# Kernel tuning notes

Measured on AMD Instinct MI355X. Metric: run time of the kernel, lower is better.

The kernel has to match this reference:

```python
import jax, jax.numpy as jnp
import numpy as np

N_USER = 100000
N_ITEM = 50000
N_NODES = N_USER + N_ITEM
LATDIM = 64
N_EDGES = 4800000
N_LAYERS = 3


def setup_inputs() -> dict:
    key = jax.random.key(0)
    k1, k2, k3, k4 = jax.random.split(key, 4)
    ini_embeds = jax.random.normal(k1, (N_NODES, LATDIM), dtype=jnp.float32)
    edge_src = jax.random.randint(k2, (N_EDGES,), 0, N_NODES, dtype=jnp.int32)
    edge_dst = jax.random.randint(k3, (N_EDGES,), 0, N_NODES, dtype=jnp.int32)
    edge_w = jax.random.uniform(k4, (N_EDGES,), dtype=jnp.float32)
    return {
        "ini_embeds": ini_embeds,
        "edge_src": edge_src,
        "edge_dst": edge_dst,
        "edge_w": edge_w,
        "n_user": N_USER,
        "n_layers": N_LAYERS,
    }


def _spmm(edge_src, edge_dst, edge_w, x, n_nodes):
    # out[dst] += w * x[src]  == adj @ x for sparse adj in COO form
    msgs = x[edge_src] * edge_w[:, None]  # [E, D]
    return jax.ops.segment_sum(msgs, edge_dst, num_segments=n_nodes)


def reference(ini_embeds, edge_src, edge_dst, edge_w, n_user, n_layers):
    n_nodes = ini_embeds.shape[0]
    embeds = ini_embeds
    acc = ini_embeds  # running sum of all layer embeddings (LightGCN layer sum)
    for _ in range(n_layers):
        embeds = _spmm(edge_src, edge_dst, edge_w, embeds, n_nodes)
        acc = acc + embeds
    return acc[:n_user], acc[n_user:]
```

## Files before the change

### kernel.cpp

```cpp
#include <hip/hip_runtime.h>
#include <hip/hip_fp16.h>


#define D 64
#define BSH 9
#define BW 512
#define PTILE 16384

#define MIXLO(acc, reg, w) \
    asm("v_fma_mix_f32 %0, %1, %2, %0 op_sel:[0,0,0] op_sel_hi:[1,0,0]" \
        : "+v"(acc) : "v"(reg), "v"(w))
#define MIXHI(acc, reg, w) \
    asm("v_fma_mix_f32 %0, %1, %2, %0 op_sel:[1,0,0] op_sel_hi:[1,0,0]" \
        : "+v"(acc) : "v"(reg), "v"(w))

__global__ __launch_bounds__(1024) void lg_tilehist(const int* __restrict__ edst,
                                                    int* __restrict__ tcnt,
                                                    int E, int NB, int ntiles,
                                                    const float* __restrict__ ini,
                                                    __half* __restrict__ h0, int n4) {
    extern __shared__ int cnt[];
    int t = blockIdx.x;
    int lo = t * PTILE;
    int hi = lo + PTILE; if (hi > E) hi = E;
    for (int i = threadIdx.x; i < NB; i += 1024) cnt[i] = 0;
    __syncthreads();
    for (int i = lo + threadIdx.x; i < hi; i += 1024)
        atomicAdd(&cnt[edst[i] >> BSH], 1);
    __syncthreads();
    for (int b = threadIdx.x; b < NB; b += 1024)
        tcnt[b * ntiles + t] = cnt[b];
    const float4* src = (const float4*)ini;
    uint2* dst = (uint2*)h0;
    int gst = gridDim.x * 1024;
    for (int i = blockIdx.x * 1024 + threadIdx.x; i < n4; i += gst) {
        float4 v = src[i];
        __half2 a = __floats2half2_rn(v.x, v.y);
        __half2 b = __floats2half2_rn(v.z, v.w);
        uint2 u;
        u.x = *reinterpret_cast<unsigned int*>(&a);
        u.y = *reinterpret_cast<unsigned int*>(&b);
        dst[i] = u;
    }
}

__global__ __launch_bounds__(1024) void lg_scan1(const int* __restrict__ tcnt,
                                                 int* __restrict__ tbase,
                                                 int* __restrict__ blksum, int NT) {
    __shared__ int lds[1024];
    int tid = threadIdx.x;
    int i = blockIdx.x * 1024 + tid;
    int v = (i < NT) ? tcnt[i] : 0;
    lds[tid] = v;
    __syncthreads();
    for (int off = 1; off < 1024; off <<= 1) {
        int t = (tid >= off) ? lds[tid - off] : 0;
        __syncthreads();
        lds[tid] += t;
        __syncthreads();
    }
    if (i < NT) tbase[i] = lds[tid] - v;
    if (tid == 1023) blksum[blockIdx.x] = lds[tid];
}

__global__ __launch_bounds__(128) void lg_scan2(int* __restrict__ blksum, int nblk,
                                                int* __restrict__ rowptr, int n_nodes, int E) {
    __shared__ int lds[128];
    int tid = threadIdx.x;
    int v = (tid < nblk) ? blksum[tid] : 0;
    lds[tid] = v;
    __syncthreads();
    for (int off = 1; off < 128; off <<= 1) {
        int t = (tid >= off) ? lds[tid - off] : 0;
        __syncthreads();
        lds[tid] += t;
        __syncthreads();
    }
    if (tid < nblk) blksum[tid] = lds[tid] - v;
    if (tid == 0) rowptr[n_nodes] = E;
}

__global__ __launch_bounds__(1024) void lg_scatter2(const int* __restrict__ esrc,
                                                    const int* __restrict__ edst,
                                                    const float* __restrict__ ew,
                                                    const int* __restrict__ tbase,
                                                    const int* __restrict__ blksum,
                                                    int2* __restrict__ bbuf,
                                                    int E, int NB, int ntiles) {
    extern __shared__ int cur[];
    int t = blockIdx.x;
    int lo = t * PTILE;
    int hi = lo + PTILE; if (hi > E) hi = E;
    for (int b = threadIdx.x; b < NB; b += 1024) {
        int idx = b * ntiles + t;
        cur[b] = tbase[idx] + blksum[idx >> 10];
    }
    __syncthreads();
    for (int i = lo + threadIdx.x; i < hi; i += 1024) {
        int d = edst[i];
        int b = d >> BSH;
        int p = atomicAdd(&cur[b], 1);
        bbuf[p] = make_int2(esrc[i] | ((d & (BW - 1)) << 18), __float_as_int(ew[i]));
    }
}

__global__ __launch_bounds__(1024) void lg_bfinal(const int2* __restrict__ bbuf,
                                                  const int* __restrict__ tbase,
                                                  const int* __restrict__ blksum,
                                                  unsigned int* __restrict__ edata,
                                                  int* __restrict__ rowptr,
                                                  int n_nodes, int NB, int ntiles, int E) {
    __shared__ int cnt[BW];
    __shared__ int cur[BW];
    __shared__ int psum[BW];
    int b = blockIdx.x;
    int i0 = b * ntiles;
    int s = tbase[i0] + blksum[i0 >> 10];
    int e;
    if (b == NB - 1) e = E;
    else { int i1 = (b + 1) * ntiles; e = tbase[i1] + blksum[i1 >> 10]; }
    int tid = threadIdx.x;
    if (tid < BW) cnt[tid] = 0;
    __syncthreads();
    for (int i = s + tid; i < e; i += 1024)
        atomicAdd(&cnt[((unsigned)bbuf[i].x >> 18) & (BW - 1)], 1);
    __syncthreads();
    if (tid < BW) psum[tid] = cnt[tid];
    __syncthreads();
    for (int off = 1; off < BW; off <<= 1) {
        int v = 0;
        if (tid < BW && tid >= off) v = psum[tid - off];
        __syncthreads();
        if (tid < BW) psum[tid] += v;
        __syncthreads();
    }
    if (tid < BW) {
        int excl = psum[tid] - cnt[tid];
        cur[tid] = excl;
        int node = b * BW + tid;
        if (node < n_nodes) rowptr[node] = s + excl;
    }
    __syncthreads();
    for (int i = s + tid; i < e; i += 1024) {
        int2 ed = bbuf[i];
        int loc = ((unsigned)ed.x >> 18) & (BW - 1);
        int p = s + atomicAdd(&cur[loc], 1);
        unsigned int src = (unsigned)(ed.x & 0x3FFFF);
        float w = __int_as_float(ed.y);
        unsigned int wq = (unsigned int)(w * 16384.f + 0.5f);
        if (wq > 16383u) wq = 16383u;
        edata[p] = (src << 14) | wq;
    }
}

template <bool FIRST, bool LAST>
__global__ __launch_bounds__(256) void lg_gather(const unsigned int* __restrict__ edata,
                                                 const int* __restrict__ rowptr,
                                                 const __half* __restrict__ x,
                                                 __half* __restrict__ y,
                                                 float* __restrict__ acc,
                                                 const float* __restrict__ ini,
                                                 int n_nodes) {
    int wid = (blockIdx.x * blockDim.x + threadIdx.x) >> 6;
    int lane = threadIdx.x & 63;
    if (wid >= n_nodes) return;
    int o = lane >> 3, c = lane & 7;
    int start = rowptr[wid], end = rowptr[wid + 1];
    float a0 = 0.f, a1 = 0.f, a2 = 0.f, a3 = 0.f;
    float a4 = 0.f, a5 = 0.f, a6 = 0.f, a7 = 0.f;
    const float kInv = 1.f / 16384.f;
    int base = start;
    for (; base + 16 <= end; base += 16) {
        unsigned int r0 = edata[base + o];
        unsigned int r1 = edata[base + 8 + o];
        uint4 u0 = *((const uint4*)(x + ((size_t)(r0 >> 14) << 6)) + c);
        uint4 u1 = *((const uint4*)(x + ((size_t)(r1 >> 14) << 6)) + c);
        float w0 = (float)(r0 & 16383u) * kInv;
        float w1 = (float)(r1 & 16383u) * kInv;
        MIXLO(a0, u0.x, w0); MIXHI(a1, u0.x, w0);
        MIXLO(a2, u0.y, w0); MIXHI(a3, u0.y, w0);
        MIXLO(a4, u0.z, w0); MIXHI(a5, u0.z, w0);
        MIXLO(a6, u0.w, w0); MIXHI(a7, u0.w, w0);
        MIXLO(a0, u1.x, w1); MIXHI(a1, u1.x, w1);
        MIXLO(a2, u1.y, w1); MIXHI(a3, u1.y, w1);
        MIXLO(a4, u1.z, w1); MIXHI(a5, u1.z, w1);
        MIXLO(a6, u1.w, w1); MIXHI(a7, u1.w, w1);
    }
    for (; base < end; base += 8) {
        int idx = base + o;
        if (idx < end) {
            unsigned int r0 = edata[idx];
            uint4 u0 = *((const uint4*)(x + ((size_t)(r0 >> 14) << 6)) + c);
            float w0 = (float)(r0 & 16383u) * kInv;
            MIXLO(a0, u0.x, w0); MIXHI(a1, u0.x, w0);
            MIXLO(a2, u0.y, w0); MIXHI(a3, u0.y, w0);
            MIXLO(a4, u0.z, w0); MIXHI(a5, u0.z, w0);
            MIXLO(a6, u0.w, w0); MIXHI(a7, u0.w, w0);
        }
    }
    a0 += __shfl_xor(a0, 8); a0 += __shfl_xor(a0, 16); a0 += __shfl_xor(a0, 32);
    a1 += __shfl_xor(a1, 8); a1 += __shfl_xor(a1, 16); a1 += __shfl_xor(a1, 32);
    a2 += __shfl_xor(a2, 8); a2 += __shfl_xor(a2, 16); a2 += __shfl_xor(a2, 32);
    a3 += __shfl_xor(a3, 8); a3 += __shfl_xor(a3, 16); a3 += __shfl_xor(a3, 32);
    a4 += __shfl_xor(a4, 8); a4 += __shfl_xor(a4, 16); a4 += __shfl_xor(a4, 32);
    a5 += __shfl_xor(a5, 8); a5 += __shfl_xor(a5, 16); a5 += __shfl_xor(a5, 32);
    a6 += __shfl_xor(a6, 8); a6 += __shfl_xor(a6, 16); a6 += __shfl_xor(a6, 32);
    a7 += __shfl_xor(a7, 8); a7 += __shfl_xor(a7, 16); a7 += __shfl_xor(a7, 32);
    if (lane < 8) {
        size_t o32 = (size_t)wid * D + (size_t)c * 8;
        if (!LAST) {
            __half2 h0 = __floats2half2_rn(a0, a1);
            __half2 h1 = __floats2half2_rn(a2, a3);
            __half2 h2 = __floats2half2_rn(a4, a5);
            __half2 h3 = __floats2half2_rn(a6, a7);
            uint4 u;
            u.x = *reinterpret_cast<unsigned int*>(&h0);
            u.y = *reinterpret_cast<unsigned int*>(&h1);
            u.z = *reinterpret_cast<unsigned int*>(&h2);
            u.w = *reinterpret_cast<unsigned int*>(&h3);
            *((uint4*)(y + (size_t)wid * D) + c) = u;
        }
        const float* rsrc = FIRST ? (ini + o32) : (acc + o32);
        float4 r0 = *(const float4*)(rsrc);
        float4 r1 = *(const float4*)(rsrc + 4);
        *(float4*)(acc + o32)     = make_float4(r0.x + a0, r0.y + a1, r0.z + a2, r0.w + a3);
        *(float4*)(acc + o32 + 4) = make_float4(r1.x + a4, r1.y + a5, r1.z + a6, r1.w + a7);
    }
}

__global__ void lg_init_kernel(const float* __restrict__ ini, float* __restrict__ cur,
                               float* __restrict__ acc, float* __restrict__ nxt, int n4) {
    int i = blockIdx.x * blockDim.x + threadIdx.x;
    int stride = gridDim.x * blockDim.x;
    const float4* s = (const float4*)ini;
    float4* c = (float4*)cur; float4* a = (float4*)acc; float4* z = (float4*)nxt;
    float4 zero = make_float4(0.f, 0.f, 0.f, 0.f);
    for (; i < n4; i += stride) { float4 v = s[i]; c[i] = v; a[i] = v; z[i] = zero; }
}

__global__ void lg_spmm_kernel(const int* __restrict__ esrc, const int* __restrict__ edst,
                               const float* __restrict__ ew, const float* __restrict__ x,
                               float* __restrict__ y, int E) {
    int tid = blockIdx.x * blockDim.x + threadIdx.x;
    int e = tid >> 4;
    if (e >= E) return;
    int l = (tid & 15) << 2;
    int s = esrc[e]; int d = edst[e]; float w = ew[e];
    float4 v = *(const float4*)(x + s * D + l);
    float* yp = y + d * D + l;
    unsafeAtomicAdd(yp + 0, w * v.x);
    unsafeAtomicAdd(yp + 1, w * v.y);
    unsafeAtomicAdd(yp + 2, w * v.z);
    unsafeAtomicAdd(yp + 3, w * v.w);
}

__global__ void lg_addzero_kernel(float* __restrict__ acc, const float* __restrict__ nxt,
                                  float* __restrict__ zbuf, int n4) {
    int i = blockIdx.x * blockDim.x + threadIdx.x;
    int stride = gridDim.x * blockDim.x;
    float4* a = (float4*)acc; const float4* n = (const float4*)nxt; float4* z = (float4*)zbuf;
    float4 zero = make_float4(0.f, 0.f, 0.f, 0.f);
    for (; i < n4; i += stride) {
        float4 av = a[i]; float4 nv = n[i];
        av.x += nv.x; av.y += nv.y; av.z += nv.z; av.w += nv.w;
        a[i] = av; z[i] = zero;
    }
}

extern "C" void kernel_launch(void* const* d_in, const int* in_sizes, int n_in,
                              void* d_out, int out_size, void* d_ws, size_t ws_size,
                              hipStream_t stream) {
    const float* ini  = (const float*)d_in[0];
    const int*   esrc = (const int*)d_in[1];
    const int*   edst = (const int*)d_in[2];
    const float* ew   = (const float*)d_in[3];

    int n_nodes = in_sizes[0] / D;
    int E       = in_sizes[1];
    int NB      = (n_nodes + BW - 1) >> BSH;
    int ntiles  = (E + PTILE - 1) / PTILE;
    int NT      = NB * ntiles;
    int nscan   = (NT + 1023) / 1024;

    size_t hBytes     = ((size_t)n_nodes * D * sizeof(__half) + 255) & ~(size_t)255;
    size_t epackBytes = (((size_t)E * 4) + 255) & ~(size_t)255;
    size_t bbufBytes  = (size_t)E * sizeof(int2);
    size_t ptrBytes   = (((size_t)n_nodes + 1) * 4 + 15) & ~(size_t)15;
    size_t tcntBytes  = (((size_t)NT * 4) + 15) & ~(size_t)15;
    size_t blkBytes   = (128 * 4 + 15) & ~(size_t)15;
    size_t need = 2 * hBytes + epackBytes + bbufBytes + ptrBytes + 2 * tcntBytes + blkBytes + 64;

    float* acc = (float*)d_out;

    if (ws_size >= need && nscan <= 128) {
        char* p = (char*)d_ws;
        __half* h0    = (__half*)p; p += hBytes;
        __half* h1    = (__half*)p; p += hBytes;
        unsigned int* edata = (unsigned int*)p; p += epackBytes;
        int2*  bbuf   = (int2*)p;   p += bbufBytes;
        int*   rowptr = (int*)p;    p += ptrBytes;
        int*   tcnt   = (int*)p;    p += tcntBytes;
        int*   tbase  = (int*)p;    p += tcntBytes;
        int*   blksum = (int*)p;

        int n4 = n_nodes * D / 4;

        lg_tilehist<<<ntiles, 1024, (size_t)NB * 4, stream>>>(edst, tcnt, E, NB, ntiles,
                                                              ini, h0, n4);
        lg_scan1<<<nscan, 1024, 0, stream>>>(tcnt, tbase, blksum, NT);
        lg_scan2<<<1, 128, 0, stream>>>(blksum, nscan, rowptr, n_nodes, E);
        lg_scatter2<<<ntiles, 1024, (size_t)NB * 4, stream>>>(esrc, edst, ew, tbase, blksum,
                                                              bbuf, E, NB, ntiles);
        lg_bfinal<<<NB, 1024, 0, stream>>>(bbuf, tbase, blksum, edata, rowptr,
                                           n_nodes, NB, ntiles, E);

        int gblocks = (int)(((size_t)n_nodes * 64 + 255) / 256);
        lg_gather<true,  false><<<gblocks, 256, 0, stream>>>(edata, rowptr, h0, h1, acc, ini, n_nodes);
        lg_gather<false, false><<<gblocks, 256, 0, stream>>>(edata, rowptr, h1, h0, acc, ini, n_nodes);
        lg_gather<false, true ><<<gblocks, 256, 0, stream>>>(edata, rowptr, h0, h1, acc, ini, n_nodes);
    } else {
        int n4 = (n_nodes * D) / 4;
        float* cur = (float*)d_ws;
        float* nxt = cur + (size_t)n_nodes * D;
        lg_init_kernel<<<2048, 256, 0, stream>>>(ini, cur, acc, nxt, n4);
        int spmm_blocks = (E * 16 + 255) / 256;
        for (int layer = 0; layer < 3; ++layer) {
            lg_spmm_kernel<<<spmm_blocks, 256, 0, stream>>>(esrc, edst, ew, cur, nxt, E);
            lg_addzero_kernel<<<2048, 256, 0, stream>>>(acc, nxt, cur, n4);
            float* t = cur; cur = nxt; nxt = t;
        }
    }
}
```

Baseline: 393.0 us.

## Split fp16 embeddings into four column-chunk planes and defer accumulation to final pass

The fp16 embedding buffers become chunk-major: four planes of 16 columns each. Each gather block handles one plane for four nodes, so a random-gather working set is a quarter of the table and fits better in cache. Interleaving the pass index in the block id spreads the planes across concurrent blocks. The per-layer fp32 acc read-modify-write is dropped: layer outputs are kept in separate fp16 buffers (one reuses the bucket scratch) and summed once in a final kernel, at the cost of a third buffer and an extra launch.

```diff
diff --git a/kernel.cpp b/kernel.cpp
--- a/kernel.cpp
+++ b/kernel.cpp
@@ -32,15 +32,17 @@
         tcnt[b * ntiles + t] = cnt[b];
     const float4* src = (const float4*)ini;
     uint2* dst = (uint2*)h0;
+    int n_nodes = n4 >> 4;
     int gst = gridDim.x * 1024;
     for (int i = blockIdx.x * 1024 + threadIdx.x; i < n4; i += gst) {
         float4 v = src[i];
+        int node = i >> 4, q = i & 15, c = q >> 2, ofs = q & 3;
         __half2 a = __floats2half2_rn(v.x, v.y);
         __half2 b = __floats2half2_rn(v.z, v.w);
         uint2 u;
         u.x = *reinterpret_cast<unsigned int*>(&a);
         u.y = *reinterpret_cast<unsigned int*>(&b);
-        dst[i] = u;
+        dst[(((size_t)c * n_nodes + node) << 2) + ofs] = u;
     }
 }
 
@@ -153,78 +155,80 @@
     }
 }
 
-template <bool FIRST, bool LAST>
-__global__ __launch_bounds__(256) void lg_gather(const unsigned int* __restrict__ edata,
-                                                 const int* __restrict__ rowptr,
-                                                 const __half* __restrict__ x,
-                                                 __half* __restrict__ y,
-                                                 float* __restrict__ acc,
-                                                 const float* __restrict__ ini,
-                                                 int n_nodes) {
-    int wid = (blockIdx.x * blockDim.x + threadIdx.x) >> 6;
+__global__ __launch_bounds__(256) void lg_gather4(const unsigned int* __restrict__ edata,
+                                                  const int* __restrict__ rowptr,
+                                                  const __half* __restrict__ x,
+                                                  __half* __restrict__ y,
+                                                  int n_nodes) {
+    int b = blockIdx.x;
+    int pass = b & 3;
+    int node = (b >> 2) * 4 + (threadIdx.x >> 6);
+    if (node >= n_nodes) return;
     int lane = threadIdx.x & 63;
-    if (wid >= n_nodes) return;
-    int o = lane >> 3, c = lane & 7;
-    int start = rowptr[wid], end = rowptr[wid + 1];
+    int o = lane >> 2, c = lane & 3;
+    const __half* xp = x + ((size_t)pass * n_nodes) * 16;
+    int start = rowptr[node], end = rowptr[node + 1];
     float a0 = 0.f, a1 = 0.f, a2 = 0.f, a3 = 0.f;
-    float a4 = 0.f, a5 = 0.f, a6 = 0.f, a7 = 0.f;
     const float kInv = 1.f / 16384.f;
     int base = start;
-    for (; base + 16 <= end; base += 16) {
+    for (; base + 32 <= end; base += 32) {
         unsigned int r0 = edata[base + o];
-        unsigned int r1 = edata[base + 8 + o];
-        uint4 u0 = *((const uint4*)(x + ((size_t)(r0 >> 14) << 6)) + c);
-        uint4 u1 = *((const uint4*)(x + ((size_t)(r1 >> 14) << 6)) + c);
+        unsigned int r1 = edata[base + 16 + o];
+        uint2 u0 = *((const uint2*)(xp + ((size_t)(r0 >> 14) << 4)) + c);
+        uint2 u1 = *((const uint2*)(xp + ((size_t)(r1 >> 14) << 4)) + c);
         float w0 = (float)(r0 & 16383u) * kInv;
         float w1 = (float)(r1 & 16383u) * kInv;
         MIXLO(a0, u0.x, w0); MIXHI(a1, u0.x, w0);
         MIXLO(a2, u0.y, w0); MIXHI(a3, u0.y, w0);
-        MIXLO(a4, u0.z, w0); MIXHI(a5, u0.z, w0);
-        MIXLO(a6, u0.w, w0); MIXHI(a7, u0.w, w0);
         MIXLO(a0, u1.x, w1); MIXHI(a1, u1.x, w1);
         MIXLO(a2, u1.y, w1); MIXHI(a3, u1.y, w1);
-        MIXLO(a4, u1.z, w1); MIXHI(a5, u1.z, w1);
-        MIXLO(a6, u1.w, w1); MIXHI(a7, u1.w, w1);
-    }
-    for (; base < end; base += 8) {
+    }
+    for (; base < end; base += 16) {
         int idx = base + o;
         if (idx < end) {
             unsigned int r0 = edata[idx];
-            uint4 u0 = *((const uint4*)(x + ((size_t)(r0 >> 14) << 6)) + c);
+            uint2 u0 = *((const uint2*)(xp + ((size_t)(r0 >> 14) << 4)) + c);
             float w0 = (float)(r0 & 16383u) * kInv;
             MIXLO(a0, u0.x, w0); MIXHI(a1, u0.x, w0);
             MIXLO(a2, u0.y, w0); MIXHI(a3, u0.y, w0);
-            MIXLO(a4, u0.z, w0); MIXHI(a5, u0.z, w0);
-            MIXLO(a6, u0.w, w0); MIXHI(a7, u0.w, w0);
         }
     }
-    a0 += __shfl_xor(a0, 8); a0 += __shfl_xor(a0, 16); a0 += __shfl_xor(a0, 32);
-    a1 += __shfl_xor(a1, 8); a1 += __shfl_xor(a1, 16); a1 += __shfl_xor(a1, 32);
-    a2 += __shfl_xor(a2, 8); a2 += __shfl_xor(a2, 16); a2 += __shfl_xor(a2, 32);
-    a3 += __shfl_xor(a3, 8); a3 += __shfl_xor(a3, 16); a3 += __shfl_xor(a3, 32);
-    a4 += __shfl_xor(a4, 8); a4 += __shfl_xor(a4, 16); a4 += __shfl_xor(a4, 32);
-    a5 += __shfl_xor(a5, 8); a5 += __shfl_xor(a5, 16); a5 += __shfl_xor(a5, 32);
-    a6 += __shfl_xor(a6, 8); a6 += __shfl_xor(a6, 16); a6 += __shfl_xor(a6, 32);
-    a7 += __shfl_xor(a7, 8); a7 += __shfl_xor(a7, 16); a7 += __shfl_xor(a7, 32);
-    if (lane < 8) {
-        size_t o32 = (size_t)wid * D + (size_t)c * 8;
-        if (!LAST) {
-            __half2 h0 = __floats2half2_rn(a0, a1);
-            __half2 h1 = __floats2half2_rn(a2, a3);
-            __half2 h2 = __floats2half2_rn(a4, a5);
-            __half2 h3 = __floats2half2_rn(a6, a7);
-            uint4 u;
-            u.x = *reinterpret_cast<unsigned int*>(&h0);
-            u.y = *reinterpret_cast<unsigned int*>(&h1);
-            u.z = *reinterpret_cast<unsigned int*>(&h2);
-            u.w = *reinterpret_cast<unsigned int*>(&h3);
-            *((uint4*)(y + (size_t)wid * D) + c) = u;
-        }
-        const float* rsrc = FIRST ? (ini + o32) : (acc + o32);
-        float4 r0 = *(const float4*)(rsrc);
-        float4 r1 = *(const float4*)(rsrc + 4);
-        *(float4*)(acc + o32)     = make_float4(r0.x + a0, r0.y + a1, r0.z + a2, r0.w + a3);
-        *(float4*)(acc + o32 + 4) = make_float4(r1.x + a4, r1.y + a5, r1.z + a6, r1.w + a7);
+    a0 += __shfl_xor(a0, 4); a0 += __shfl_xor(a0, 8); a0 += __shfl_xor(a0, 16); a0 += __shfl_xor(a0, 32);
+    a1 += __shfl_xor(a1, 4); a1 += __shfl_xor(a1, 8); a1 += __shfl_xor(a1, 16); a1 += __shfl_xor(a1, 32);
+    a2 += __shfl_xor(a2, 4); a2 += __shfl_xor(a2, 8); a2 += __shfl_xor(a2, 16); a2 += __shfl_xor(a2, 32);
+    a3 += __shfl_xor(a3, 4); a3 += __shfl_xor(a3, 8); a3 += __shfl_xor(a3, 16); a3 += __shfl_xor(a3, 32);
+    if (lane < 4) {
+        __half2 h0 = __floats2half2_rn(a0, a1);
+        __half2 h1 = __floats2half2_rn(a2, a3);
+        uint2 u;
+        u.x = *reinterpret_cast<unsigned int*>(&h0);
+        u.y = *reinterpret_cast<unsigned int*>(&h1);
+        *((uint2*)(y + ((size_t)pass * n_nodes + node) * 16) + lane) = u;
+    }
+}
+
+__global__ void lg_final(const float* __restrict__ ini,
+                         const __half* __restrict__ y1,
+                         const __half* __restrict__ y2,
+                         const __half* __restrict__ y3,
+                         float* __restrict__ out, int n_nodes) {
+    int tot = n_nodes * 16;
+    int st = gridDim.x * blockDim.x;
+    for (int i = blockIdx.x * blockDim.x + threadIdx.x; i < tot; i += st) {
+        int node = i >> 4, q = i & 15, c = q >> 2, ofs = q & 3;
+        size_t yidx = (((size_t)c * n_nodes + node) << 2) + ofs;
+        float4 r = ((const float4*)ini)[i];
+        uint2 u1 = ((const uint2*)y1)[yidx];
+        uint2 u2 = ((const uint2*)y2)[yidx];
+        uint2 u3 = ((const uint2*)y3)[yidx];
+        float2 f;
+        f = __half22float2(*reinterpret_cast<__half2*>(&u1.x)); r.x += f.x; r.y += f.y;
+        f = __half22float2(*reinterpret_cast<__half2*>(&u1.y)); r.z += f.x; r.w += f.y;
+        f = __half22float2(*reinterpret_cast<__half2*>(&u2.x)); r.x += f.x; r.y += f.y;
+        f = __half22float2(*reinterpret_cast<__half2*>(&u2.y)); r.z += f.x; r.w += f.y;
+        f = __half22float2(*reinterpret_cast<__half2*>(&u3.x)); r.x += f.x; r.y += f.y;
+        f = __half22float2(*reinterpret_cast<__half2*>(&u3.y)); r.z += f.x; r.w += f.y;
+        ((float4*)out)[i] = r;
     }
 }
 
@@ -284,11 +288,11 @@
 
     size_t hBytes     = ((size_t)n_nodes * D * sizeof(__half) + 255) & ~(size_t)255;
     size_t epackBytes = (((size_t)E * 4) + 255) & ~(size_t)255;
-    size_t bbufBytes  = (size_t)E * sizeof(int2);
+    size_t bbufBytes  = ((size_t)E * sizeof(int2) + 255) & ~(size_t)255;
     size_t ptrBytes   = (((size_t)n_nodes + 1) * 4 + 15) & ~(size_t)15;
     size_t tcntBytes  = (((size_t)NT * 4) + 15) & ~(size_t)15;
     size_t blkBytes   = (128 * 4 + 15) & ~(size_t)15;
-    size_t need = 2 * hBytes + epackBytes + bbufBytes + ptrBytes + 2 * tcntBytes + blkBytes + 64;
+    size_t need = 3 * hBytes + epackBytes + bbufBytes + ptrBytes + 2 * tcntBytes + blkBytes + 64;
 
     float* acc = (float*)d_out;
 
@@ -296,12 +300,14 @@
         char* p = (char*)d_ws;
         __half* h0    = (__half*)p; p += hBytes;
         __half* h1    = (__half*)p; p += hBytes;
+        __half* h2    = (__half*)p; p += hBytes;
         unsigned int* edata = (unsigned int*)p; p += epackBytes;
         int2*  bbuf   = (int2*)p;   p += bbufBytes;
         int*   rowptr = (int*)p;    p += ptrBytes;
         int*   tcnt   = (int*)p;    p += tcntBytes;
         int*   tbase  = (int*)p;    p += tcntBytes;
         int*   blksum = (int*)p;
+        __half* h3    = (__half*)bbuf;
 
         int n4 = n_nodes * D / 4;
 
@@ -314,10 +320,11 @@
         lg_bfinal<<<NB, 1024, 0, stream>>>(bbuf, tbase, blksum, edata, rowptr,
                                            n_nodes, NB, ntiles, E);
 
-        int gblocks = (int)(((size_t)n_nodes * 64 + 255) / 256);
-        lg_gather<true,  false><<<gblocks, 256, 0, stream>>>(edata, rowptr, h0, h1, acc, ini, n_nodes);
-        lg_gather<false, false><<<gblocks, 256, 0, stream>>>(edata, rowptr, h1, h0, acc, ini, n_nodes);
-        lg_gather<false, true ><<<gblocks, 256, 0, stream>>>(edata, rowptr, h0, h1, acc, ini, n_nodes);
+        int gblocks = ((n_nodes + 3) / 4) * 4;
+        lg_gather4<<<gblocks, 256, 0, stream>>>(edata, rowptr, h0, h1, n_nodes);
+        lg_gather4<<<gblocks, 256, 0, stream>>>(edata, rowptr, h1, h2, n_nodes);
+        lg_gather4<<<gblocks, 256, 0, stream>>>(edata, rowptr, h2, h3, n_nodes);
+        lg_final<<<2048, 256, 0, stream>>>(ini, h1, h2, h3, acc, n_nodes);
     } else {
         int n4 = (n_nodes * D) / 4;
         float* cur = (float*)d_ws;
```

Result: slower. 713.8 us (+81.6%).
